# Performance work log

Measured on AMD Instinct MI355X. Metric: run time of the kernel, lower is better.

## Reference

```python
import jax, jax.numpy as jnp
import numpy as np

# ---- parameters (mirror torch module init) ----
DT = 1e-3            # clock_sim
T = 500              # tot_time / clock_sim
BS = 256             # trials_per_stimulus
N = 256              # neurons_n
# LIF (oscillator)
C_OSC = 1e-3; THR_OSC = 1.0; TAU_SYN = 5e-3; TAU_NEU = 1e-2
GAIN_SYN = 1e-3; VR_OSC = 0.0; REFR_OSC = 0.002 / DT
I_MIN = 0.12; I_STEP = 2e-4
# TDE
C_TDE = 1e-3; THR_TDE = 1.0; TAU_TRG = 1e-2; TAU_FAC = 5e-3
GAIN_FAC = 1.0; GAIN_TRG = 2.0; IFAC_THR = 0.1; BETA = 1e-2
VR_TDE = 0.0; REFR_TDE = 0.002 / DT
SCALE = 20.0  # SurrGradSpike.scale


@jax.custom_vjp
def spike(x):
    return (x > 0.0).astype(x.dtype)

def _spike_fwd(x):
    return spike(x), x

def _spike_bwd(x, g):
    return (g / (SCALE * jnp.abs(x) + 1.0) ** 2,)

spike.defvjp(_spike_fwd, _spike_bwd)


def setup_inputs() -> dict:
    key = jax.random.key(0)
    k1, _ = jax.random.split(key)
    # per-trial input spike train, (T, BS), Bernoulli(0.1)
    inp = (jax.random.uniform(k1, (T, BS)) < 0.1).astype(jnp.float32)
    # learnable current list (linspace as in sPLL.__init__)
    current_list = jnp.linspace(I_MIN, I_MIN + I_STEP * N, N, dtype=jnp.float32)
    return {"input": inp, "current_list": current_list}


def reference(input, current_list):
    steady = jnp.broadcast_to(current_list[None, :], (BS, N))  # LIF steady current

    def step(carry, inp_t):
        Vl, Il, crl, Vt, itrg, ifac, crt, spk_tde_prev = carry
        # expand per-trial input spike across all N neurons: (BS,) -> (BS, N)
        x = jnp.broadcast_to(inp_t[:, None], (BS, N))
        # ---- LIF step (driven by previous TDE spikes) ----
        Il = Il * (1.0 - DT / TAU_SYN) + GAIN_SYN * spk_tde_prev
        Vl = Vl + DT * (-Vl / TAU_NEU + (Il + steady) / C_OSC)
        spk_l = spike(Vl - THR_OSC)
        crl = REFR_OSC * spk_l + (1.0 - spk_l) * (crl - 1.0)
        Vl = (1.0 - spk_l) * Vl * (crl <= 0.0).astype(Vl.dtype) + spk_l * VR_OSC
        # ---- TDE step (trg = external input, fac = LIF spikes) ----
        ifac = spk_l * GAIN_FAC + ifac * (1.0 - spk_l)
        ifac = ifac * (1.0 - DT / TAU_FAC)
        itrg = itrg * (1.0 - DT / TAU_TRG)
        itrg = itrg + x * GAIN_TRG * ifac * (ifac > IFAC_THR).astype(ifac.dtype)
        Vt = Vt + DT * (-Vt / BETA + itrg / C_TDE)
        spk_t = spike(Vt - THR_TDE)
        crt = REFR_TDE * spk_t + (1.0 - spk_t) * (crt - 1.0)
        Vt = (1.0 - spk_t) * Vt * (crt <= 0.0).astype(Vt.dtype) + spk_t * VR_TDE
        return (Vl, Il, crl, Vt, itrg, ifac, crt, spk_t), (spk_l, spk_t)

    z = jnp.zeros((BS, N), dtype=jnp.float32)
    init = (jnp.ones((BS, N), dtype=jnp.float32), z, z,  # LIF: V=1, I=0, cr=0
            z, z, z, z,                                   # TDE: V, i_trg, i_fac, cr
            z)                                            # spikes_TDE_prev
    _, (spk_lif, spk_tde) = jax.lax.scan(step, init, input)
    return jnp.stack([spk_lif, spk_tde])  # (2, T, BS, N)
```

## Files before the change

### kernel.cpp

```cpp
#include <hip/hip_runtime.h>

static constexpr int T     = 500;
static constexpr int BS    = 256;
static constexpr int N     = 256;
static constexpr int U     = 10;
static constexpr int SPLIT = 380;

#define FPBAR(x) asm("" : "+v"(x))

__device__ __forceinline__ void do_step(
    float x, float steady,
    float& Vl, float& Il, float& crl,
    float& Vt, float& itrg, float& ifac, float& crt,
    bool& sp_b, float& sl_out, float& st_out)
{
    const float RC = 999.99993896484375f;

    float u0 = Il * 0.8f;                     FPBAR(u0);
    float u1 = sp_b ? 1e-3f : 0.0f;
    Il = u0 + u1;                             FPBAR(Il);
    float u3 = -Vl * 100.0f;                  FPBAR(u3);
    float u4 = Il + steady;                   FPBAR(u4);
    float u6 = __builtin_fmaf(u4, RC, u3);    FPBAR(u6);
    Vl = __builtin_fmaf(1e-3f, u6, Vl);       FPBAR(Vl);
    float dvl = Vl - 1.0f;                    FPBAR(dvl);
    bool  bl  = dvl > 0.0f;
    float crm = crl - 1.0f;
    bool  rg  = crm <= 0.0f;
    crl = bl ? 2.0f : crm;
    Vl  = bl ? 0.0f : (rg ? Vl : 0.0f);
    sl_out = bl ? 1.0f : 0.0f;

    float u13 = bl ? 1.0f : ifac;
    ifac = u13 * 0.8f;                        FPBAR(ifac);
    float w0 = itrg * 0.9f;                   FPBAR(w0);
    float df  = ifac + ifac;
    float dfx = x * df;                       FPBAR(dfx);
    bool  m1  = ifac > 0.1f;
    float pulse = m1 ? dfx : 0.0f;
    itrg = w0 + pulse;                        FPBAR(itrg);
    float u18 = -Vt * 100.0f;                 FPBAR(u18);
    float u20 = __builtin_fmaf(itrg, RC, u18); FPBAR(u20);
    Vt = __builtin_fmaf(1e-3f, u20, Vt);      FPBAR(Vt);
    float dvt = Vt - 1.0f;                    FPBAR(dvt);
    bool  bt  = dvt > 0.0f;
    float ctm = crt - 1.0f;
    bool  rg2 = ctm <= 0.0f;
    crt = bt ? 2.0f : ctm;
    Vt  = bt ? 0.0f : (rg2 ? Vt : 0.0f);
    st_out = bt ? 1.0f : 0.0f;
    sp_b = bt;
}

struct Cell {
    float Vl, Il, crl, Vt, itrg, ifac, crt;
    bool  sp;
};

template <bool STORE>
__device__ __forceinline__ void run_group(
    const float* __restrict__ s_inp, int g, float steady, Cell& c,
    float*& p0, float*& p1, size_t step)
{
    const float2 x01 = *reinterpret_cast<const float2*>(&s_inp[g * U + 0]);
    const float2 x23 = *reinterpret_cast<const float2*>(&s_inp[g * U + 2]);
    const float2 x45 = *reinterpret_cast<const float2*>(&s_inp[g * U + 4]);
    const float2 x67 = *reinterpret_cast<const float2*>(&s_inp[g * U + 6]);
    const float2 x89 = *reinterpret_cast<const float2*>(&s_inp[g * U + 8]);
    const float xs[U] = {x01.x, x01.y, x23.x, x23.y, x45.x,
                         x45.y, x67.x, x67.y, x89.x, x89.y};
    float sl, st;
#pragma unroll
    for (int j = 0; j < U; ++j) {
        do_step(xs[j], steady, c.Vl, c.Il, c.crl, c.Vt, c.itrg, c.ifac, c.crt,
                c.sp, sl, st);
        if (STORE) {
            p0[(size_t)j * step] = sl;
            p1[(size_t)j * step] = st;
        }
    }
    if (STORE) {
        p0 += (size_t)U * step;
        p1 += (size_t)U * step;
    }
}

__global__ __launch_bounds__(256, 2) void spll_kernel(
    const float* __restrict__ inp,
    const float* __restrict__ current,
    float* __restrict__ out)
{
#pragma clang fp contract(off)
    const int b    = blockIdx.x & (BS - 1);
    const int role = blockIdx.x >> 8;
    const int n    = threadIdx.x;

    __shared__ __align__(16) float s_inp[T];
    for (int i = threadIdx.x; i < T; i += blockDim.x)
        s_inp[i] = inp[i * BS + b];
    __syncthreads();

    const float steady = current[n];

    Cell c = {1.0f, 0.0f, 0.0f, 0.0f, 0.0f, 0.0f, 0.0f, false};

    float* p0 = out + (size_t)b * N + n;
    float* p1 = p0 + (size_t)T * BS * N;
    const size_t step = (size_t)BS * N;

    if (role == 0) {
        for (int g = 0; g < SPLIT / U; ++g)
            run_group<true>(s_inp, g, steady, c, p0, p1, step);
    } else {
        p0 += (size_t)SPLIT * step;
        p1 += (size_t)SPLIT * step;
        for (int g = 0; g < SPLIT / U; ++g)
            run_group<false>(s_inp, g, steady, c, p0, p1, step);
        for (int g = SPLIT / U; g < T / U; ++g)
            run_group<true>(s_inp, g, steady, c, p0, p1, step);
    }
}

extern "C" void kernel_launch(void* const* d_in, const int* in_sizes, int n_in,
                              void* d_out, int out_size, void* d_ws, size_t ws_size,
                              hipStream_t stream) {
    const float* a0 = (const float*)d_in[0];
    const float* a1 = (const float*)d_in[1];
    const float* inp = a0;
    const float* cur = a1;
    if (n_in >= 2 && in_sizes[0] == N && in_sizes[1] == T * BS) { inp = a1; cur = a0; }
    float* out = (float*)d_out;
    spll_kernel<<<dim3(2 * BS), dim3(N), 0, stream>>>(inp, cur, out);
}
```

Before: 54.98 us.

## Split time range across four redundant-recompute roles instead of two

```diff
diff --git a/kernel.cpp b/kernel.cpp
--- a/kernel.cpp
+++ b/kernel.cpp
@@ -1,61 +1,57 @@
 #include <hip/hip_runtime.h>
 
-static constexpr int T     = 500;
-static constexpr int BS    = 256;
-static constexpr int N     = 256;
-static constexpr int U     = 10;
-static constexpr int SPLIT = 380;
+static constexpr int T  = 500;
+static constexpr int BS = 256;
+static constexpr int N  = 256;
+static constexpr int U  = 10;
+static constexpr int R  = 4;
+__constant__ __device__ const int CS[R + 1] = {0, 120, 250, 370, 500};
 
 #define FPBAR(x) asm("" : "+v"(x))
-
-__device__ __forceinline__ void do_step(
-    float x, float steady,
-    float& Vl, float& Il, float& crl,
-    float& Vt, float& itrg, float& ifac, float& crt,
-    bool& sp_b, float& sl_out, float& st_out)
-{
-    const float RC = 999.99993896484375f;
-
-    float u0 = Il * 0.8f;                     FPBAR(u0);
-    float u1 = sp_b ? 1e-3f : 0.0f;
-    Il = u0 + u1;                             FPBAR(Il);
-    float u3 = -Vl * 100.0f;                  FPBAR(u3);
-    float u4 = Il + steady;                   FPBAR(u4);
-    float u6 = __builtin_fmaf(u4, RC, u3);    FPBAR(u6);
-    Vl = __builtin_fmaf(1e-3f, u6, Vl);       FPBAR(Vl);
-    float dvl = Vl - 1.0f;                    FPBAR(dvl);
-    bool  bl  = dvl > 0.0f;
-    float crm = crl - 1.0f;
-    bool  rg  = crm <= 0.0f;
-    crl = bl ? 2.0f : crm;
-    Vl  = bl ? 0.0f : (rg ? Vl : 0.0f);
-    sl_out = bl ? 1.0f : 0.0f;
-
-    float u13 = bl ? 1.0f : ifac;
-    ifac = u13 * 0.8f;                        FPBAR(ifac);
-    float w0 = itrg * 0.9f;                   FPBAR(w0);
-    float df  = ifac + ifac;
-    float dfx = x * df;                       FPBAR(dfx);
-    bool  m1  = ifac > 0.1f;
-    float pulse = m1 ? dfx : 0.0f;
-    itrg = w0 + pulse;                        FPBAR(itrg);
-    float u18 = -Vt * 100.0f;                 FPBAR(u18);
-    float u20 = __builtin_fmaf(itrg, RC, u18); FPBAR(u20);
-    Vt = __builtin_fmaf(1e-3f, u20, Vt);      FPBAR(Vt);
-    float dvt = Vt - 1.0f;                    FPBAR(dvt);
-    bool  bt  = dvt > 0.0f;
-    float ctm = crt - 1.0f;
-    bool  rg2 = ctm <= 0.0f;
-    crt = bt ? 2.0f : ctm;
-    Vt  = bt ? 0.0f : (rg2 ? Vt : 0.0f);
-    st_out = bt ? 1.0f : 0.0f;
-    sp_b = bt;
-}
 
 struct Cell {
     float Vl, Il, crl, Vt, itrg, ifac, crt;
     bool  sp;
 };
+
+__device__ __forceinline__ void do_step(
+    float x, float steady, Cell& c, float& sl_out, float& st_out)
+{
+    const float RC = 999.99993896484375f;
+
+    float u0 = c.Il * 0.8f;                      FPBAR(u0);
+    float u1 = c.sp ? 1e-3f : 0.0f;
+    c.Il = u0 + u1;                              FPBAR(c.Il);
+    float u3 = -c.Vl * 100.0f;                   FPBAR(u3);
+    float u4 = c.Il + steady;                    FPBAR(u4);
+    float u6 = __builtin_fmaf(u4, RC, u3);       FPBAR(u6);
+    c.Vl = __builtin_fmaf(1e-3f, u6, c.Vl);      FPBAR(c.Vl);
+    bool  bl  = c.Vl > 1.0f;
+    float crm = c.crl - 1.0f;
+    bool  rg  = crm <= 0.0f;
+    c.crl = bl ? 2.0f : crm;
+    c.Vl  = (!bl && rg) ? c.Vl : 0.0f;
+    sl_out = bl ? 1.0f : 0.0f;
+
+    float u13 = bl ? 1.0f : c.ifac;
+    c.ifac = u13 * 0.8f;                         FPBAR(c.ifac);
+    float w0 = c.itrg * 0.9f;                    FPBAR(w0);
+    float df  = c.ifac + c.ifac;
+    float dfx = x * df;                          FPBAR(dfx);
+    bool  m1  = c.ifac > 0.1f;
+    float pulse = m1 ? dfx : 0.0f;
+    c.itrg = w0 + pulse;                         FPBAR(c.itrg);
+    float u18 = -c.Vt * 100.0f;                  FPBAR(u18);
+    float u20 = __builtin_fmaf(c.itrg, RC, u18); FPBAR(u20);
+    c.Vt = __builtin_fmaf(1e-3f, u20, c.Vt);     FPBAR(c.Vt);
+    bool  bt  = c.Vt > 1.0f;
+    float ctm = c.crt - 1.0f;
+    bool  rg2 = ctm <= 0.0f;
+    c.crt = bt ? 2.0f : ctm;
+    c.Vt  = (!bt && rg2) ? c.Vt : 0.0f;
+    st_out = bt ? 1.0f : 0.0f;
+    c.sp = bt;
+}
 
 template <bool STORE>
 __device__ __forceinline__ void run_group(
@@ -72,8 +68,7 @@
     float sl, st;
 #pragma unroll
     for (int j = 0; j < U; ++j) {
-        do_step(xs[j], steady, c.Vl, c.Il, c.crl, c.Vt, c.itrg, c.ifac, c.crt,
-                c.sp, sl, st);
+        do_step(xs[j], steady, c, sl, st);
         if (STORE) {
             p0[(size_t)j * step] = sl;
             p1[(size_t)j * step] = st;
@@ -85,7 +80,7 @@
     }
 }
 
-__global__ __launch_bounds__(256, 2) void spll_kernel(
+__global__ __launch_bounds__(256, 4) void spll_kernel(
     const float* __restrict__ inp,
     const float* __restrict__ current,
     float* __restrict__ out)
@@ -104,21 +99,17 @@
 
     Cell c = {1.0f, 0.0f, 0.0f, 0.0f, 0.0f, 0.0f, 0.0f, false};
 
-    float* p0 = out + (size_t)b * N + n;
+    const int gs = CS[role] / U;
+    const int ge = CS[role + 1] / U;
+
+    float* p0 = out + (size_t)b * N + n + (size_t)CS[role] * BS * N;
     float* p1 = p0 + (size_t)T * BS * N;
     const size_t step = (size_t)BS * N;
 
-    if (role == 0) {
-        for (int g = 0; g < SPLIT / U; ++g)
-            run_group<true>(s_inp, g, steady, c, p0, p1, step);
-    } else {
-        p0 += (size_t)SPLIT * step;
-        p1 += (size_t)SPLIT * step;
-        for (int g = 0; g < SPLIT / U; ++g)
-            run_group<false>(s_inp, g, steady, c, p0, p1, step);
-        for (int g = SPLIT / U; g < T / U; ++g)
-            run_group<true>(s_inp, g, steady, c, p0, p1, step);
-    }
+    for (int g = 0; g < gs; ++g)
+        run_group<false>(s_inp, g, steady, c, p0, p1, step);
+    for (int g = gs; g < ge; ++g)
+        run_group<true>(s_inp, g, steady, c, p0, p1, step);
 }
 
 extern "C" void kernel_launch(void* const* d_in, const int* in_sizes, int n_in,
@@ -130,5 +121,5 @@
     const float* cur = a1;
     if (n_in >= 2 && in_sizes[0] == N && in_sizes[1] == T * BS) { inp = a1; cur = a0; }
     float* out = (float*)d_out;
-    spll_kernel<<<dim3(2 * BS), dim3(N), 0, stream>>>(inp, cur, out);
+    spll_kernel<<<dim3(R * BS), dim3(N), 0, stream>>>(inp, cur, out);
 }
```

Measured after the change: 61.89 us. 12.6% more time.
